# Performance work log

Measured on AMD Instinct MI355X. Metric: run time of the kernel, lower is better.

Reference implementation:

```python
import jax, jax.numpy as jnp
import numpy as np
import math

NUM_BANDS = 16
BINS = 1024
CROPSIZE = 1024
BATCH = 4


def setup_inputs() -> dict:
    key = jax.random.key(0)
    ks = jax.random.split(key, 10)
    s = 1.0 / math.sqrt(BINS)
    return {
        "x": jax.random.normal(ks[0], (BATCH, CROPSIZE, BINS), jnp.float32),
        "Wq": jax.random.normal(ks[1], (BINS, BINS), jnp.float32) * s,
        "bq": jax.random.normal(ks[2], (BINS,), jnp.float32) * 0.02,
        "Wk": jax.random.normal(ks[3], (BINS, BINS), jnp.float32) * s,
        "bk": jax.random.normal(ks[4], (BINS,), jnp.float32) * 0.02,
        "Wv": jax.random.normal(ks[5], (BINS, BINS), jnp.float32) * s,
        "bv": jax.random.normal(ks[6], (BINS,), jnp.float32) * 0.02,
        "Wo": jax.random.normal(ks[7], (BINS, BINS), jnp.float32) * s,
        "bo": jax.random.normal(ks[8], (BINS,), jnp.float32) * 0.02,
        "er": jax.random.normal(ks[9], (BINS // NUM_BANDS, CROPSIZE), jnp.float32),
    }


def reference(x, Wq, bq, Wk, bk, Wv, bv, Wo, bo, er):
    b, w, c = x.shape
    h = NUM_BANDS
    d = c // h
    # Linear projections (torch Linear: x @ W.T + b)
    q = (jnp.einsum("bwc,oc->bwo", x, Wq) + bq).reshape(b, w, h, d).transpose(0, 2, 1, 3)  # [b,h,w,d]
    k = (jnp.einsum("bwc,oc->bwo", x, Wk) + bk).reshape(b, w, h, d).transpose(0, 2, 1, 3)  # [b,h,w,d]
    v = (jnp.einsum("bwc,oc->bwo", x, Wv) + bv).reshape(b, w, h, d).transpose(0, 2, 1, 3)  # [b,h,w,d]
    # relative-position bias via skew trick
    qe = jnp.einsum("bhwd,dc->bhwc", q, er)  # [b,h,w,cropsize]
    qe = jnp.pad(qe, ((0, 0), (0, 0), (0, 0), (1, 0)))  # pad last dim on left -> [b,h,w,crop+1]
    p = jnp.swapaxes(qe, 2, 3)[:, :, 1:, :]  # [b,h,crop,w] == [b,h,w,w] since crop==w
    qk = (jnp.einsum("bhwd,bhud->bhwu", q, k) + p) / math.sqrt(c)
    a = jax.nn.softmax(qk, axis=-1)
    av = jnp.einsum("bhwu,bhud->bhwd", a, v).transpose(0, 2, 1, 3).reshape(b, w, c)
    return jnp.einsum("bwc,oc->bwo", av, Wo) + bo
```

## Files before the change

kernel.cpp:

```cpp
#include <hip/hip_runtime.h>
#include <stdint.h>

typedef __attribute__((ext_vector_type(8))) short   short8;
typedef __attribute__((ext_vector_type(8))) __bf16  bf16x8;
typedef __attribute__((ext_vector_type(4))) float   floatx4;

__device__ __forceinline__ float bf2f(uint16_t h) {
    union { uint32_t u; float f; } v; v.u = ((uint32_t)h) << 16; return v.f;
}
__device__ __forceinline__ uint16_t f2bf(float f) {
    union { float f; uint32_t u; } v; v.f = f;
    uint32_t u = v.u;
    u += 0x7FFFu + ((u >> 16) & 1u);
    return (uint16_t)(u >> 16);
}
__device__ __forceinline__ floatx4 mfma16(short8 a, short8 b, floatx4 c) {
    return __builtin_amdgcn_mfma_f32_16x16x32_bf16(
        __builtin_bit_cast(bf16x8, a), __builtin_bit_cast(bf16x8, b), c, 0, 0, 0);
}
__device__ __forceinline__ void gll16(const short* g, short* l) {
    __builtin_amdgcn_global_load_lds(
        (const __attribute__((address_space(1))) uint32_t*)g,
        (__attribute__((address_space(3))) uint32_t*)l, 16, 0, 0);
}

__global__ void conv_all(
    const float* __restrict__ x,
    const float* __restrict__ Wq, const float* __restrict__ Wk,
    const float* __restrict__ Wv, const float* __restrict__ Wo,
    const float* __restrict__ bq, const float* __restrict__ bk,
    const float* __restrict__ bv, const float* __restrict__ bo,
    const float* __restrict__ er,
    short* __restrict__ xb, short* __restrict__ Wb,
    short* __restrict__ ball, short* __restrict__ ErT)
{
    int blk = blockIdx.x, tid = threadIdx.x;
    if (blk < 4096) {
        int i = blk * 256 + tid;
        float4 v = ((const float4*)x)[i];
        ((short4*)xb)[i] = make_short4((short)f2bf(v.x), (short)f2bf(v.y),
                                       (short)f2bf(v.z), (short)f2bf(v.w));
    } else if (blk < 8192) {
        int rel = blk - 4096;
        int wsel = rel >> 10;
        int i = (rel & 1023) * 256 + tid;
        const float* W = (wsel == 0) ? Wq : (wsel == 1) ? Wk : (wsel == 2) ? Wv : Wo;
        float4 v = ((const float4*)W)[i];
        ((short4*)(Wb + ((size_t)wsel << 20)))[i] =
            make_short4((short)f2bf(v.x), (short)f2bf(v.y),
                        (short)f2bf(v.z), (short)f2bf(v.w));
    } else if (blk < 8448) {
        int idx = (blk - 8192) * 256 + tid;
        int w = idx >> 6, d = idx & 63;
        ErT[idx] = (short)f2bf(er[d * 1024 + w]);
    } else {
        int idx = (blk - 8448) * 256 + tid;
        int sel = idx >> 10, j = idx & 1023;
        const float* s = (sel == 0) ? bq : (sel == 1) ? bk : (sel == 2) ? bv : bo;
        ball[idx] = (short)f2bf(s[j]);
    }
}

__device__ __forceinline__ void gemm_body(
    const short* __restrict__ A, const short* __restrict__ Wt,
    const short* __restrict__ bias, short* __restrict__ dst,
    float* __restrict__ dstf, int variant)
{
    __shared__ short As[128 * 64];
    __shared__ short Bs[128 * 64];
    const int tid  = threadIdx.x;
    const int wid  = tid >> 6;
    const int lane = tid & 63;
    const int m0 = blockIdx.x * 128;
    const int n0 = blockIdx.y * 128;
    const int wm = (wid >> 1) * 64;
    const int wn = (wid & 1) * 64;
    const int lrow = lane & 15;
    const int quad = lane >> 4;
    const int srow = lane >> 3;
    const int sscol = (((lane & 7) ^ (srow & 7)) << 3);
    const int rx = lrow & 7;

    floatx4 acc[4][4];
#pragma unroll
    for (int r = 0; r < 4; ++r)
#pragma unroll
        for (int c = 0; c < 4; ++c) acc[r][c] = (floatx4){0.f, 0.f, 0.f, 0.f};

    for (int k0 = 0; k0 < 1024; k0 += 64) {
#pragma unroll
        for (int i = 0; i < 4; ++i) {
            int q = wid * 4 + i;
            gll16(A + (size_t)(m0 + q * 8 + srow) * 1024 + k0 + sscol,
                  &As[q * 512 + lane * 8]);
        }
#pragma unroll
        for (int i = 0; i < 4; ++i) {
            int q = wid * 4 + i;
            gll16(Wt + (size_t)(n0 + q * 8 + srow) * 1024 + k0 + sscol,
                  &Bs[q * 512 + lane * 8]);
        }
        __syncthreads();
#pragma unroll
        for (int ks = 0; ks < 2; ++ks) {
            short8 af[4], bfr[4];
#pragma unroll
            for (int r = 0; r < 4; ++r)
                af[r] = *(const short8*)&As[(wm + r * 16 + lrow) * 64 +
                                            (((ks * 4 + quad) ^ rx) << 3)];
#pragma unroll
            for (int c = 0; c < 4; ++c)
                bfr[c] = *(const short8*)&Bs[(wn + c * 16 + lrow) * 64 +
                                             (((ks * 4 + quad) ^ rx) << 3)];
#pragma unroll
            for (int r = 0; r < 4; ++r)
#pragma unroll
                for (int c = 0; c < 4; ++c)
                    acc[r][c] = mfma16(af[r], bfr[c], acc[r][c]);
        }
        __syncthreads();
    }

#pragma unroll
    for (int c = 0; c < 4; ++c) {
        int col = n0 + wn + c * 16 + lrow;
        float bv = bf2f((uint16_t)bias[col]);
#pragma unroll
        for (int r = 0; r < 4; ++r) {
#pragma unroll
            for (int g = 0; g < 4; ++g) {
                int m = m0 + wm + r * 16 + quad * 4 + g;
                float fv = acc[r][c][g] + bv;
                if (variant == 3) {
                    dstf[(size_t)m * 1024 + col] = fv;
                } else if (variant == 2) {
                    int bh = (m >> 10) * 16 + (col >> 6);
                    dst[(size_t)bh * 65536 + (size_t)(col & 63) * 1024 + (m & 1023)] =
                        (short)f2bf(fv);
                } else {
                    int bh = (m >> 10) * 16 + (col >> 6);
                    dst[(size_t)bh * 65536 + (size_t)(m & 1023) * 64 + (col & 63)] =
                        (short)f2bf(fv);
                }
            }
        }
    }
}

__global__ __launch_bounds__(256) void out_gemm(
    const short* __restrict__ AV, const short* __restrict__ Wo,
    const short* __restrict__ bo, float* __restrict__ out)
{
    gemm_body(AV, Wo, bo, nullptr, out, 3);
}

#define VM7  asm volatile("s_waitcnt vmcnt(7)" ::: "memory")
#define VM6  asm volatile("s_waitcnt vmcnt(6)" ::: "memory")
#define VM0  asm volatile("s_waitcnt vmcnt(0)" ::: "memory")
#define BARR asm volatile("s_barrier" ::: "memory")

__device__ __forceinline__ void stage_unit(const short* src, short* region, int tid)
{
    const int row  = tid >> 3;
    const int scol = (((tid & 7) ^ (row & 7)) << 3);
    gll16(src + (size_t)row * 1024 + scol, region + tid * 8);
}

#define SAU(buf, u) (As + (buf) * 16384 + (u) * 4096)
#define SBU(buf, u) (Bs + (buf) * 12288 + (u) * 4096)
#define STG_A(buf, u, kt) stage_unit(Asrc + (size_t)(u) * 65536 + (size_t)(kt) * 64, SAU(buf, u), tid)
#define STG_B(buf, u, kt) stage_unit(Bsrc + (size_t)(u) * 65536 + (size_t)(kt) * 64, SBU(buf, u), tid)

#define RD_A(buf) do { \
    _Pragma("unroll") for (int fr_ = 0; fr_ < 8; ++fr_) { \
        const short* p_ = SAU(buf, wm * 2 + (fr_ >> 2)) + ((fr_ & 3) * 16 + lrow) * 64; \
        _Pragma("unroll") for (int ks_ = 0; ks_ < 2; ++ks_) \
            a[fr_][ks_] = *(const short8*)&p_[((ks_ * 4 + quad) ^ rx) << 3]; \
    } } while (0)

#define RD_B(buf, c) do { \
    const short* p_ = SBU(buf, c) + (wn * 16 + lrow) * 64; \
    _Pragma("unroll") for (int ks_ = 0; ks_ < 2; ++ks_) \
        bb[ks_] = *(const short8*)&p_[((ks_ * 4 + quad) ^ rx) << 3]; \
    } while (0)

#define MFMA_PH(c) do { \
    __builtin_amdgcn_s_setprio(1); \
    _Pragma("unroll") for (int ks_ = 0; ks_ < 2; ++ks_) \
        _Pragma("unroll") for (int fr_ = 0; fr_ < 8; ++fr_) \
            acc[fr_][c] = mfma16(a[fr_][ks_], bb[ks_], acc[fr_][c]); \
    __builtin_amdgcn_s_setprio(0); \
    } while (0)

__global__ __launch_bounds__(512, 2) void qkv_gemm192(
    const short* __restrict__ x, const short* __restrict__ Wb,
    const short* __restrict__ ball,
    short* __restrict__ Qb, short* __restrict__ Kb, short* __restrict__ Vb)
{
    extern __shared__ short lds[];
    short* As = lds;
    short* Bs = lds + 32768;
    const int tid  = threadIdx.x;
    const int wid  = tid >> 6;
    const int lane = tid & 63;
    const int wm   = wid >> 2;
    const int wn   = wid & 3;
    const int lrow = lane & 15;
    const int quad = lane >> 4;
    const int rx   = lrow & 7;
    const int bid  = blockIdx.x;
    const int swz  = (bid & 7) * 32 + (bid >> 3);
    const int mi   = swz & 15, ni = swz >> 4;
    const int m0   = mi * 256, n0 = ni * 192;
    const short* Asrc = x  + (size_t)m0 * 1024;
    const short* Bsrc = Wb + (size_t)n0 * 1024;

    floatx4 acc[8][3];
#pragma unroll
    for (int r = 0; r < 8; ++r)
#pragma unroll
        for (int c = 0; c < 3; ++c) acc[r][c] = (floatx4){0.f, 0.f, 0.f, 0.f};

    short8 a[8][2], bb[2];

    STG_A(0, 0, 0); STG_A(0, 1, 0); STG_A(0, 2, 0); STG_A(0, 3, 0);
    STG_B(0, 0, 0); STG_B(0, 1, 0); STG_B(0, 2, 0);
    STG_A(1, 0, 1); STG_A(1, 1, 1); STG_A(1, 2, 1); STG_A(1, 3, 1);
    STG_B(1, 0, 1); STG_B(1, 1, 1);
    VM6; BARR;

#pragma unroll 1
    for (int i = 0; i < 7; ++i) {
        const int t1 = 2 * i + 1, s0 = 2 * i + 2, s1 = 2 * i + 3;
        STG_B(1, 2, t1);
        VM7; BARR;
        RD_A(0); RD_B(0, 0); MFMA_PH(0);
        BARR;
        STG_A(0, 0, s0); STG_A(0, 1, s0); STG_B(0, 0, s0);
        BARR; RD_B(0, 1); MFMA_PH(1); BARR;
        STG_A(0, 2, s0); STG_A(0, 3, s0); STG_B(0, 1, s0);
        BARR; RD_B(0, 2); MFMA_PH(2); BARR;
        STG_B(0, 2, s0);
        VM7; BARR;
        RD_A(1); RD_B(1, 0); MFMA_PH(0);
        BARR;
        STG_A(1, 0, s1); STG_A(1, 1, s1); STG_B(1, 0, s1);
        BARR; RD_B(1, 1); MFMA_PH(1); BARR;
        STG_A(1, 2, s1); STG_A(1, 3, s1); STG_B(1, 1, s1);
        BARR; RD_B(1, 2); MFMA_PH(2); BARR;
    }

    STG_B(1, 2, 15);
    VM7; BARR;
    RD_A(0); RD_B(0, 0); MFMA_PH(0);
    RD_B(0, 1); MFMA_PH(1);
    RD_B(0, 2); MFMA_PH(2);
    VM0; BARR;
    RD_A(1); RD_B(1, 0); MFMA_PH(0);
    RD_B(1, 1); MFMA_PH(1);
    RD_B(1, 2); MFMA_PH(2);

#pragma unroll
    for (int fc = 0; fc < 3; ++fc) {
        int col = n0 + fc * 64 + wn * 16 + lrow;
        int z   = col >> 10;
        int c1  = col & 1023;
        short* dst = (z == 0) ? Qb : (z == 1) ? Kb : Vb;
        float bv = bf2f((uint16_t)ball[col]);
#pragma unroll
        for (int fr = 0; fr < 8; ++fr) {
#pragma unroll
            for (int g = 0; g < 4; ++g) {
                int m = m0 + wm * 128 + fr * 16 + quad * 4 + g;
                float fv = acc[fr][fc][g] + bv;
                int bh = (m >> 10) * 16 + (c1 >> 6);
                if (z == 2)
                    dst[(size_t)bh * 65536 + (size_t)(c1 & 63) * 1024 + (m & 1023)] =
                        (short)f2bf(fv);
                else
                    dst[(size_t)bh * 65536 + (size_t)(m & 1023) * 64 + (c1 & 63)] =
                        (short)f2bf(fv);
            }
        }
    }
}

#define PSTR 72
__global__ __launch_bounds__(512) void attn_kernel(
    const short* __restrict__ Q, const short* __restrict__ K,
    const short* __restrict__ Vt, const short* __restrict__ ErT,
    short* __restrict__ AV)
{
    __shared__ short Ks [2][64 * 64];
    __shared__ short Qks[2][64 * 64];
    __shared__ short Vs [2][64 * 64];
    __shared__ short Ps [128 * PSTR];
    const int tid  = threadIdx.x;
    const int wid  = tid >> 6;
    const int lane = tid & 63;
    const int lrow = lane & 15;
    const int quad = lane >> 4;
    const int lk   = quad * 8;
    const int srow = lane >> 3;
    const int sscol = (((lane & 7) ^ (srow & 7)) << 3);
    const int rx = lrow & 7;
    const int h = blockIdx.x, b = blockIdx.y;
    const int bh = b * 16 + h;
    const int i0 = blockIdx.z * 128;
    const int wrow = wid * 16;
    const short* Qbh = Q  + (size_t)bh * 65536;
    const short* Kbh = K  + (size_t)bh * 65536;
    const short* Vbh = Vt + (size_t)bh * 65536;

    short8 qa[4];
    {
        int row = i0 + wrow + lrow;
#pragma unroll
        for (int kk = 0; kk < 2; ++kk) {
            qa[kk]     = *(const short8*)&Qbh[(size_t)row * 64 + kk * 32 + lk];
            qa[kk + 2] = *(const short8*)&ErT[(size_t)row * 64 + kk * 32 + lk];
        }
    }

    float lrun[4];
    floatx4 oacc[4];
#pragma unroll
    for (int g = 0; g < 4; ++g) lrun[g] = 0.f;
#pragma unroll
    for (int c = 0; c < 4; ++c) oacc[c] = (floatx4){0.f, 0.f, 0.f, 0.f};

    {
        gll16(Kbh + (size_t)(wid * 8 + srow) * 64 + sscol,    &Ks [0][wid * 512 + lane * 8]);
        gll16(Qbh + (size_t)(wid * 8 + srow) * 64 + sscol,    &Qks[0][wid * 512 + lane * 8]);
        gll16(Vbh + (size_t)(wid * 8 + srow) * 1024 + sscol,  &Vs [0][wid * 512 + lane * 8]);
    }

    const float sc2 = 1.44269504088896f / 32.0f;

    for (int jt = 0; jt < 16; ++jt) {
        const int cur = jt & 1;
        __syncthreads();

        if (jt < 15) {
            int j1 = (jt + 1) * 64;
            gll16(Kbh + (size_t)(j1 + wid * 8 + srow) * 64 + sscol,    &Ks [cur ^ 1][wid * 512 + lane * 8]);
            gll16(Qbh + (size_t)(j1 + wid * 8 + srow) * 64 + sscol,    &Qks[cur ^ 1][wid * 512 + lane * 8]);
            gll16(Vbh + (size_t)(wid * 8 + srow) * 1024 + j1 + sscol,  &Vs [cur ^ 1][wid * 512 + lane * 8]);
        }

        floatx4 s[4];
#pragma unroll
        for (int c = 0; c < 4; ++c) s[c] = (floatx4){0.f, 0.f, 0.f, 0.f};
#pragma unroll
        for (int kk = 0; kk < 4; ++kk) {
            short8 kb[4];
#pragma unroll
            for (int c = 0; c < 4; ++c) {
                int kl = (kk < 2) ? kk : kk - 2;
                const short* src = (kk < 2) ? Ks[cur] : Qks[cur];
                kb[c] = *(const short8*)&src[(c * 16 + lrow) * 64 +
                                             (((kl * 4 + quad) ^ rx) << 3)];
            }
#pragma unroll
            for (int c = 0; c < 4; ++c)
                s[c] = mfma16(qa[kk], kb[c], s[c]);
        }

#pragma unroll
        for (int c = 0; c < 4; ++c)
#pragma unroll
            for (int g = 0; g < 4; ++g)
                s[c][g] = exp2f(s[c][g] * sc2);
#pragma unroll
        for (int g = 0; g < 4; ++g) {
            float rs = (s[0][g] + s[1][g]) + (s[2][g] + s[3][g]);
#pragma unroll
            for (int d = 1; d < 16; d <<= 1) rs += __shfl_xor(rs, d, 64);
            lrun[g] += rs;
        }

#pragma unroll
        for (int c = 0; c < 4; ++c)
#pragma unroll
            for (int g = 0; g < 4; ++g)
                Ps[(wrow + quad * 4 + g) * PSTR + c * 16 + lrow] = (short)f2bf(s[c][g]);
        __asm__ __volatile__("" ::: "memory");

#pragma unroll
        for (int kk = 0; kk < 2; ++kk) {
            short8 pa, vb[4];
            pa = *(const short8*)&Ps[(wrow + lrow) * PSTR + kk * 32 + lk];
#pragma unroll
            for (int c = 0; c < 4; ++c)
                vb[c] = *(const short8*)&Vs[cur][(c * 16 + lrow) * 64 +
                                                 (((kk * 4 + quad) ^ rx) << 3)];
#pragma unroll
            for (int c = 0; c < 4; ++c)
                oacc[c] = mfma16(pa, vb[c], oacc[c]);
        }
    }

#pragma unroll
    for (int c = 0; c < 4; ++c)
#pragma unroll
        for (int g = 0; g < 4; ++g) {
            int row = i0 + wrow + quad * 4 + g;
            int colc = h * 64 + c * 16 + lrow;
            AV[((size_t)b * 1024 + row) * 1024 + colc] = (short)f2bf(oacc[c][g] / lrun[g]);
        }
}

extern "C" void kernel_launch(void* const* d_in, const int* in_sizes, int n_in,
                              void* d_out, int out_size, void* d_ws, size_t ws_size,
                              hipStream_t stream) {
    const float* x  = (const float*)d_in[0];
    const float* Wq = (const float*)d_in[1];
    const float* bq = (const float*)d_in[2];
    const float* Wk = (const float*)d_in[3];
    const float* bk = (const float*)d_in[4];
    const float* Wv = (const float*)d_in[5];
    const float* bv = (const float*)d_in[6];
    const float* Wo = (const float*)d_in[7];
    const float* bo = (const float*)d_in[8];
    const float* er = (const float*)d_in[9];
    float* out = (float*)d_out;

    const size_t M1 = 1u << 20;
    short* ws   = (short*)d_ws;
    short* xb   = (short*)d_out;
    short* Qb   = ws;
    short* Kb   = ws + 4 * M1;
    short* Vb   = ws + 8 * M1;
    short* AVb  = ws + 12 * M1;
    short* Wb   = ws + 16 * M1;
    short* ball = ws + 20 * M1;
    short* ErT  = ws + 20 * M1 + 4096;

    static bool attr_done = false;
    if (!attr_done) {
        hipFuncSetAttribute((const void*)qkv_gemm192,
                            hipFuncAttributeMaxDynamicSharedMemorySize, 114688);
        attr_done = true;
    }

    hipLaunchKernelGGL(conv_all, dim3(8464), dim3(256), 0, stream,
                       x, Wq, Wk, Wv, Wo, bq, bk, bv, bo, er, xb, Wb, ball, ErT);
    hipLaunchKernelGGL(qkv_gemm192, dim3(256), dim3(512), 114688, stream,
                       xb, Wb, ball, Qb, Kb, Vb);
    hipLaunchKernelGGL(attn_kernel, dim3(16, 4, 8), dim3(512), 0, stream,
                       Qb, Kb, Vb, ErT, AVb);
    hipLaunchKernelGGL(out_gemm, dim3(32, 8), dim3(256), 0, stream,
                       AVb, Wb + 3 * M1, ball + 3072, out);
}
```

Before: 209.4 us.

## Split attention warps 2x2 over rows and key columns, reduce partials in LDS

Measured after the change: 201.5 us. -3.8%, faster.

```diff
diff --git a/kernel.cpp b/kernel.cpp
--- a/kernel.cpp
+++ b/kernel.cpp
@@ -286,18 +286,24 @@
 }
 
 #define PSTR 72
-__global__ __launch_bounds__(512) void attn_kernel(
+__global__ __launch_bounds__(512, 4) void attn_kernel(
     const short* __restrict__ Q, const short* __restrict__ K,
     const short* __restrict__ Vt, const short* __restrict__ ErT,
     short* __restrict__ AV)
 {
-    __shared__ short Ks [2][64 * 64];
-    __shared__ short Qks[2][64 * 64];
-    __shared__ short Vs [2][64 * 64];
-    __shared__ short Ps [128 * PSTR];
+    __shared__ short smem[33792];
+    short* Ks  = smem;
+    short* Qks = smem + 8192;
+    short* Vs  = smem + 16384;
+    short* Ps  = smem + 24576;
+    float* oaccS = (float*)smem;
+    float* lrunS = ((float*)smem) + 128 * 65;
+
     const int tid  = threadIdx.x;
     const int wid  = tid >> 6;
     const int lane = tid & 63;
+    const int rg   = wid >> 1;
+    const int cg   = wid & 1;
     const int lrow = lane & 15;
     const int quad = lane >> 4;
     const int lk   = quad * 8;
@@ -307,33 +313,34 @@
     const int h = blockIdx.x, b = blockIdx.y;
     const int bh = b * 16 + h;
     const int i0 = blockIdx.z * 128;
-    const int wrow = wid * 16;
     const short* Qbh = Q  + (size_t)bh * 65536;
     const short* Kbh = K  + (size_t)bh * 65536;
     const short* Vbh = Vt + (size_t)bh * 65536;
 
-    short8 qa[4];
-    {
-        int row = i0 + wrow + lrow;
+    short8 qa[2][4];
+#pragma unroll
+    for (int m = 0; m < 2; ++m) {
+        int row = i0 + rg * 32 + m * 16 + lrow;
 #pragma unroll
         for (int kk = 0; kk < 2; ++kk) {
-            qa[kk]     = *(const short8*)&Qbh[(size_t)row * 64 + kk * 32 + lk];
-            qa[kk + 2] = *(const short8*)&ErT[(size_t)row * 64 + kk * 32 + lk];
-        }
-    }
-
-    float lrun[4];
-    floatx4 oacc[4];
-#pragma unroll
-    for (int g = 0; g < 4; ++g) lrun[g] = 0.f;
-#pragma unroll
-    for (int c = 0; c < 4; ++c) oacc[c] = (floatx4){0.f, 0.f, 0.f, 0.f};
-
-    {
-        gll16(Kbh + (size_t)(wid * 8 + srow) * 64 + sscol,    &Ks [0][wid * 512 + lane * 8]);
-        gll16(Qbh + (size_t)(wid * 8 + srow) * 64 + sscol,    &Qks[0][wid * 512 + lane * 8]);
-        gll16(Vbh + (size_t)(wid * 8 + srow) * 1024 + sscol,  &Vs [0][wid * 512 + lane * 8]);
-    }
+            qa[m][kk]     = *(const short8*)&Qbh[(size_t)row * 64 + kk * 32 + lk];
+            qa[m][kk + 2] = *(const short8*)&ErT[(size_t)row * 64 + kk * 32 + lk];
+        }
+    }
+
+    float lrun[2][4];
+    floatx4 oacc[2][4];
+#pragma unroll
+    for (int m = 0; m < 2; ++m) {
+#pragma unroll
+        for (int g = 0; g < 4; ++g) lrun[m][g] = 0.f;
+#pragma unroll
+        for (int c = 0; c < 4; ++c) oacc[m][c] = (floatx4){0.f, 0.f, 0.f, 0.f};
+    }
+
+    gll16(Kbh + (size_t)(wid * 8 + srow) * 64 + sscol,    Ks  + wid * 512 + lane * 8);
+    gll16(Qbh + (size_t)(wid * 8 + srow) * 64 + sscol,    Qks + wid * 512 + lane * 8);
+    gll16(Vbh + (size_t)(wid * 8 + srow) * 1024 + sscol,  Vs  + wid * 512 + lane * 8);
 
     const float sc2 = 1.44269504088896f / 32.0f;
 
@@ -343,71 +350,114 @@
 
         if (jt < 15) {
             int j1 = (jt + 1) * 64;
-            gll16(Kbh + (size_t)(j1 + wid * 8 + srow) * 64 + sscol,    &Ks [cur ^ 1][wid * 512 + lane * 8]);
-            gll16(Qbh + (size_t)(j1 + wid * 8 + srow) * 64 + sscol,    &Qks[cur ^ 1][wid * 512 + lane * 8]);
-            gll16(Vbh + (size_t)(wid * 8 + srow) * 1024 + j1 + sscol,  &Vs [cur ^ 1][wid * 512 + lane * 8]);
-        }
-
-        floatx4 s[4];
-#pragma unroll
-        for (int c = 0; c < 4; ++c) s[c] = (floatx4){0.f, 0.f, 0.f, 0.f};
+            gll16(Kbh + (size_t)(j1 + wid * 8 + srow) * 64 + sscol,    Ks  + (cur ^ 1) * 4096 + wid * 512 + lane * 8);
+            gll16(Qbh + (size_t)(j1 + wid * 8 + srow) * 64 + sscol,    Qks + (cur ^ 1) * 4096 + wid * 512 + lane * 8);
+            gll16(Vbh + (size_t)(wid * 8 + srow) * 1024 + j1 + sscol,  Vs  + (cur ^ 1) * 4096 + wid * 512 + lane * 8);
+        }
+
+        floatx4 s[2][2];
+#pragma unroll
+        for (int m = 0; m < 2; ++m)
+#pragma unroll
+            for (int c = 0; c < 2; ++c) s[m][c] = (floatx4){0.f, 0.f, 0.f, 0.f};
 #pragma unroll
         for (int kk = 0; kk < 4; ++kk) {
-            short8 kb[4];
-#pragma unroll
-            for (int c = 0; c < 4; ++c) {
-                int kl = (kk < 2) ? kk : kk - 2;
-                const short* src = (kk < 2) ? Ks[cur] : Qks[cur];
-                kb[c] = *(const short8*)&src[(c * 16 + lrow) * 64 +
+            short8 kb[2];
+            const short* src = ((kk < 2) ? Ks : Qks) + cur * 4096;
+            const int kl = kk & 1;
+#pragma unroll
+            for (int c = 0; c < 2; ++c)
+                kb[c] = *(const short8*)&src[(cg * 32 + c * 16 + lrow) * 64 +
                                              (((kl * 4 + quad) ^ rx) << 3)];
+#pragma unroll
+            for (int m = 0; m < 2; ++m)
+#pragma unroll
+                for (int c = 0; c < 2; ++c)
+                    s[m][c] = mfma16(qa[m][kk], kb[c], s[m][c]);
+        }
+
+#pragma unroll
+        for (int m = 0; m < 2; ++m)
+#pragma unroll
+            for (int c = 0; c < 2; ++c)
+#pragma unroll
+                for (int g = 0; g < 4; ++g)
+                    s[m][c][g] = exp2f(s[m][c][g] * sc2);
+#pragma unroll
+        for (int m = 0; m < 2; ++m)
+#pragma unroll
+            for (int g = 0; g < 4; ++g)
+                lrun[m][g] += s[m][0][g] + s[m][1][g];
+
+#pragma unroll
+        for (int m = 0; m < 2; ++m)
+#pragma unroll
+            for (int c = 0; c < 2; ++c)
+#pragma unroll
+                for (int g = 0; g < 4; ++g)
+                    Ps[(rg * 32 + m * 16 + quad * 4 + g) * PSTR + cg * 32 + c * 16 + lrow] =
+                        (short)f2bf(s[m][c][g]);
+        __asm__ __volatile__("" ::: "memory");
+
+        {
+            short8 pa[2], vb[4];
+#pragma unroll
+            for (int m = 0; m < 2; ++m)
+                pa[m] = *(const short8*)&Ps[(rg * 32 + m * 16 + lrow) * PSTR + cg * 32 + lk];
+#pragma unroll
+            for (int c = 0; c < 4; ++c)
+                vb[c] = *(const short8*)&Vs[cur * 4096 + (c * 16 + lrow) * 64 +
+                                            (((cg * 4 + quad) ^ rx) << 3)];
+#pragma unroll
+            for (int m = 0; m < 2; ++m)
+#pragma unroll
+                for (int c = 0; c < 4; ++c)
+                    oacc[m][c] = mfma16(pa[m], vb[c], oacc[m][c]);
+        }
+    }
+
+#pragma unroll
+    for (int m = 0; m < 2; ++m)
+#pragma unroll
+        for (int g = 0; g < 4; ++g) {
+            float r = lrun[m][g];
+#pragma unroll
+            for (int d = 1; d < 16; d <<= 1) r += __shfl_xor(r, d, 64);
+            lrun[m][g] = r;
+        }
+
+    __syncthreads();
+    if (cg == 0) {
+#pragma unroll
+        for (int m = 0; m < 2; ++m) {
+#pragma unroll
+            for (int c = 0; c < 4; ++c)
+#pragma unroll
+                for (int g = 0; g < 4; ++g)
+                    oaccS[(rg * 32 + m * 16 + quad * 4 + g) * 65 + c * 16 + lrow] =
+                        oacc[m][c][g];
+            if (lrow == 0)
+#pragma unroll
+                for (int g = 0; g < 4; ++g)
+                    lrunS[rg * 32 + m * 16 + quad * 4 + g] = lrun[m][g];
+        }
+    }
+    __syncthreads();
+    if (cg == 1) {
+#pragma unroll
+        for (int m = 0; m < 2; ++m)
+#pragma unroll
+            for (int g = 0; g < 4; ++g) {
+                int row = rg * 32 + m * 16 + quad * 4 + g;
+                float lt = lrun[m][g] + lrunS[row];
+#pragma unroll
+                for (int c = 0; c < 4; ++c) {
+                    float tot = oacc[m][c][g] + oaccS[row * 65 + c * 16 + lrow];
+                    AV[((size_t)b * 1024 + i0 + row) * 1024 + h * 64 + c * 16 + lrow] =
+                        (short)f2bf(tot / lt);
+                }
             }
-#pragma unroll
-            for (int c = 0; c < 4; ++c)
-                s[c] = mfma16(qa[kk], kb[c], s[c]);
-        }
-
-#pragma unroll
-        for (int c = 0; c < 4; ++c)
-#pragma unroll
-            for (int g = 0; g < 4; ++g)
-                s[c][g] = exp2f(s[c][g] * sc2);
-#pragma unroll
-        for (int g = 0; g < 4; ++g) {
-            float rs = (s[0][g] + s[1][g]) + (s[2][g] + s[3][g]);
-#pragma unroll
-            for (int d = 1; d < 16; d <<= 1) rs += __shfl_xor(rs, d, 64);
-            lrun[g] += rs;
-        }
-
-#pragma unroll
-        for (int c = 0; c < 4; ++c)
-#pragma unroll
-            for (int g = 0; g < 4; ++g)
-                Ps[(wrow + quad * 4 + g) * PSTR + c * 16 + lrow] = (short)f2bf(s[c][g]);
-        __asm__ __volatile__("" ::: "memory");
-
-#pragma unroll
-        for (int kk = 0; kk < 2; ++kk) {
-            short8 pa, vb[4];
-            pa = *(const short8*)&Ps[(wrow + lrow) * PSTR + kk * 32 + lk];
-#pragma unroll
-            for (int c = 0; c < 4; ++c)
-                vb[c] = *(const short8*)&Vs[cur][(c * 16 + lrow) * 64 +
-                                                 (((kk * 4 + quad) ^ rx) << 3)];
-#pragma unroll
-            for (int c = 0; c < 4; ++c)
-                oacc[c] = mfma16(pa, vb[c], oacc[c]);
-        }
-    }
-
-#pragma unroll
-    for (int c = 0; c < 4; ++c)
-#pragma unroll
-        for (int g = 0; g < 4; ++g) {
-            int row = i0 + wrow + quad * 4 + g;
-            int colc = h * 64 + c * 16 + lrow;
-            AV[((size_t)b * 1024 + row) * 1024 + colc] = (short)f2bf(oacc[c][g] / lrun[g]);
-        }
+    }
 }
 
 extern "C" void kernel_launch(void* const* d_in, const int* in_sizes, int n_in,
```
